# Optimization experiments

Measured on AMD Instinct MI355X. Metric: run time of the kernel, lower is better.

## Reference

```python
import jax, jax.numpy as jnp
import numpy as np

N = 16384          # input points
F = 128            # feature dim (x is (N, 3+F))
POOL = 4           # pooling_factor
M = N // POOL      # number of FPS query points
K = 16             # num_neighbors


def setup_inputs() -> dict:
    key = jax.random.key(0)
    x = jax.random.normal(key, (N, 3 + F), dtype=jnp.float32)
    return {"x": x}


def _fps(coords, m):
    """Furthest point sampling: coords (N,3) -> m indices. Deterministic start at 0."""
    n = coords.shape[0]

    def step(carry, _):
        min_d2, last = carry
        d2 = jnp.sum((coords - coords[last]) ** 2, axis=-1)  # (N,)
        min_d2 = jnp.minimum(min_d2, d2)
        nxt = jnp.argmax(min_d2).astype(jnp.int32)
        return (min_d2, nxt), nxt

    init = (jnp.full((n,), jnp.inf, dtype=coords.dtype), jnp.int32(0))
    _, idxs = jax.lax.scan(step, init, None, length=m - 1)
    return jnp.concatenate([jnp.zeros((1,), dtype=jnp.int32), idxs])


def reference(x):
    coords = x[:, :3]                          # (N,3)
    fps_idx = _fps(coords, M)                  # (M,)
    q_points = coords[fps_idx]                 # (M,3)

    # knn neighbor query: squared distances (M,N), take K nearest
    d2 = jnp.sum((q_points[:, None, :] - coords[None, :, :]) ** 2, axis=-1)
    _, nbr_idx = jax.lax.top_k(-d2, K)         # (M,K)

    s_feats = x[nbr_idx, 3:]                   # (M,K,F) gather
    pooled = jnp.max(s_feats, axis=1)          # feat_mapping='max' -> (M,F)
    return jnp.concatenate([q_points, pooled], axis=-1)  # (M, 3+F)
```

## Files before the change

### kernel.cpp

```cpp
#include <hip/hip_runtime.h>

#define N_PTS 16384
#define ROWF  131
#define M_OUT 4096
#define KNN   16
#define FPS_T 1024

typedef unsigned long long u64;
typedef float f32x2 __attribute__((ext_vector_type(2)));

template <int CTRL, int ROW_MASK>
__device__ __forceinline__ float fmax_dpp(float v) {
  const int p = __builtin_amdgcn_update_dpp(__float_as_int(v), __float_as_int(v),
                                            CTRL, ROW_MASK, 0xf, false);
  return fmaxf(v, __int_as_float(p));
}
template <int CTRL, int ROW_MASK>
__device__ __forceinline__ unsigned umin_dpp(unsigned v) {
  const unsigned p = (unsigned)__builtin_amdgcn_update_dpp((int)v, (int)v,
                                            CTRL, ROW_MASK, 0xf, false);
  return v < p ? v : p;
}

__global__ void prep_kernel(const float* __restrict__ x,
                            float4* __restrict__ coords4) {
  const int p = blockIdx.x * blockDim.x + threadIdx.x;
  if (p < N_PTS) {
    coords4[p] = make_float4(x[p * ROWF + 0], x[p * ROWF + 1],
                             x[p * ROWF + 2], 0.0f);
  }
}

#define REP16R(F) F(15) F(14) F(13) F(12) F(11) F(10) F(9) F(8) \
                  F(7) F(6) F(5) F(4) F(3) F(2) F(1) F(0)
#define REPP(F) F(0,0,1) F(1,2,3) F(2,4,5) F(3,6,7) \
                F(4,8,9) F(5,10,11) F(6,12,13) F(7,14,15)

__global__
__attribute__((amdgpu_flat_work_group_size(FPS_T, FPS_T)))
__attribute__((amdgpu_waves_per_eu(4, 4)))
void fps_kernel(const float4* __restrict__ coords4, float* __restrict__ out) {
#pragma clang fp contract(off)
  __shared__ float    s_wmax[2][16];
  __shared__ unsigned s_arg[2][16];
  const int tid = threadIdx.x, lane = tid & 63, wid = tid >> 6;

#define FPS_DECL(t,a,b) f32x2 PX##t, PY##t, PZ##t; float md##a, md##b;
  REPP(FPS_DECL)
#undef FPS_DECL

#define FPS_INIT(t,a,b) {                                                  \
    const float4 va = coords4[(a << 10) + tid];                            \
    const float4 vb = coords4[(b << 10) + tid];                            \
    PX##t = (f32x2){va.x, vb.x};                                           \
    PY##t = (f32x2){va.y, vb.y};                                           \
    PZ##t = (f32x2){va.z, vb.z};                                           \
    md##a = __int_as_float(0x7f800000);                                    \
    md##b = __int_as_float(0x7f800000); }
  REPP(FPS_INIT)
#undef FPS_INIT

  if (lane == 63) { s_arg[0][wid] = 0xFFFFFFFFu; s_arg[1][wid] = 0xFFFFFFFFu; }

  const float4 q0 = coords4[0];
  float qx = q0.x, qy = q0.y, qz = q0.z;
  if (tid == 0) { out[0] = qx; out[1] = qy; out[2] = qz; }

  for (int s = 1; s < M_OUT; ++s) {
    const int par = s & 1;
    const f32x2 QX = {qx, qx}, QY = {qy, qy}, QZ = {qz, qz};

#define FPS_UPD(t,a,b) {                                                   \
    const f32x2 dx = PX##t - QX;                                           \
    const f32x2 dy = PY##t - QY;                                           \
    const f32x2 dz = PZ##t - QZ;                                           \
    const f32x2 xx = dx * dx;                                              \
    const f32x2 yy = dy * dy;                                              \
    const f32x2 zz = dz * dz;                                              \
    const f32x2 ss = xx + yy;                                              \
    const f32x2 d2 = ss + zz;                                              \
    md##a = fminf(md##a, d2.x);                                            \
    md##b = fminf(md##b, d2.y); }
    REPP(FPS_UPD)
#undef FPS_UPD

    const float a0 = fmaxf(fmaxf(md0,  md1),  md2);
    const float a1 = fmaxf(fmaxf(md3,  md4),  md5);
    const float a2 = fmaxf(fmaxf(md6,  md7),  md8);
    const float a3 = fmaxf(fmaxf(md9,  md10), md11);
    const float a4 = fmaxf(fmaxf(md12, md13), md14);
    const float b0 = fmaxf(fmaxf(a0, a1), a2);
    const float b1 = fmaxf(fmaxf(a3, a4), md15);
    const float m  = fmaxf(b0, b1);

    float fm = m;
    fm = fmax_dpp<0xB1,  0xf>(fm);
    fm = fmax_dpp<0x4E,  0xf>(fm);
    fm = fmax_dpp<0x141, 0xf>(fm);
    fm = fmax_dpp<0x140, 0xf>(fm);
    fm = fmax_dpp<0x142, 0xa>(fm);
    fm = fmax_dpp<0x143, 0xc>(fm);

    if (lane == 63) s_wmax[par][wid] = fm;
    __syncthreads();

    if (lane == 63) s_arg[par ^ 1][wid] = 0xFFFFFFFFu;

    float bm = s_wmax[par][lane & 15];
    bm = fmax_dpp<0xB1,  0xf>(bm);
    bm = fmax_dpp<0x4E,  0xf>(bm);
    bm = fmax_dpp<0x141, 0xf>(bm);
    bm = fmax_dpp<0x140, 0xf>(bm);

    const int mwb = __builtin_amdgcn_readlane(__float_as_int(fm), 63);
    const int mmb = __builtin_amdgcn_readfirstlane(__float_as_int(bm));
    if (mwb == mmb) {
      const float mmv = __int_as_float(mmb);
      unsigned c = 0xFFFFu;
#define FPS_SCAN(j) c = (md##j == mmv) ? (unsigned)j : c;
      REP16R(FPS_SCAN)
#undef FPS_SCAN
      unsigned nic = (unsigned)tid + (c << 10);
      nic = umin_dpp<0xB1,  0xf>(nic);
      nic = umin_dpp<0x4E,  0xf>(nic);
      nic = umin_dpp<0x141, 0xf>(nic);
      nic = umin_dpp<0x140, 0xf>(nic);
      nic = umin_dpp<0x142, 0xa>(nic);
      nic = umin_dpp<0x143, 0xc>(nic);
      if (lane == 63) s_arg[par][wid] = nic;
    }
    __syncthreads();

    unsigned av = s_arg[par][lane & 15];
    av = umin_dpp<0xB1,  0xf>(av);
    av = umin_dpp<0x4E,  0xf>(av);
    av = umin_dpp<0x141, 0xf>(av);
    av = umin_dpp<0x140, 0xf>(av);

    const int oidx = (int)av;
    const float4 wpt = coords4[oidx];
    qx = wpt.x; qy = wpt.y; qz = wpt.z;
    if (tid == 0) {
      float* orow = out + (size_t)s * ROWF;
      orow[0] = qx; orow[1] = qy; orow[2] = qz;
    }
  }
}

__global__ __launch_bounds__(256)
void knn_pool_kernel(const float* __restrict__ x,
                     const float4* __restrict__ coords4,
                     float* __restrict__ out) {
  const int lane = threadIdx.x & 63;
  const int q = blockIdx.x * 4 + (threadIdx.x >> 6);

  const float qx = out[(size_t)q * ROWF + 0];
  const float qy = out[(size_t)q * ROWF + 1];
  const float qz = out[(size_t)q * ROWF + 2];

  u64 h[KNN];
#pragma unroll
  for (int k = 0; k < KNN; ++k) h[k] = ~0ULL;

  for (int c = lane; c < N_PTS; c += 64) {
    const float4 v = coords4[c];
    const float dx = v.x - qx, dy = v.y - qy, dz = v.z - qz;
    const float d2 = __fadd_rn(__fadd_rn(__fmul_rn(dx, dx), __fmul_rn(dy, dy)),
                               __fmul_rn(dz, dz));
    const u64 e = ((u64)__float_as_uint(d2) << 32) | (unsigned)c;
    if (e < h[KNN - 1]) {
#pragma unroll
      for (int k = KNN - 1; k >= 1; --k) {
        const u64 prev = h[k - 1];
        h[k] = (e < prev) ? prev : ((e < h[k]) ? e : h[k]);
      }
      h[0] = (e < h[0]) ? e : h[0];
    }
  }

  int nbr[KNN];
#pragma unroll
  for (int rr = 0; rr < KNN; ++rr) {
    u64 best = h[0];
#pragma unroll
    for (int off = 32; off; off >>= 1) {
      const u64 o = __shfl_xor(best, off);
      best = (o < best) ? o : best;
    }
    nbr[rr] = (int)(unsigned)(best & 0xffffffffULL);
    if (h[0] == best) {
#pragma unroll
      for (int k = 0; k < KNN - 1; ++k) h[k] = h[k + 1];
      h[KNN - 1] = ~0ULL;
    }
  }

  float a0 = __int_as_float(0xff800000), a1 = a0;
#pragma unroll
  for (int rr = 0; rr < KNN; ++rr) {
    const float* row = x + (size_t)nbr[rr] * ROWF + 3;
    a0 = fmaxf(a0, row[lane]);
    a1 = fmaxf(a1, row[lane + 64]);
  }
  float* orow = out + (size_t)q * ROWF + 3;
  orow[lane] = a0;
  orow[lane + 64] = a1;
}

extern "C" void kernel_launch(void* const* d_in, const int* in_sizes, int n_in,
                              void* d_out, int out_size, void* d_ws, size_t ws_size,
                              hipStream_t stream) {
  const float* x = (const float*)d_in[0];
  float* out = (float*)d_out;

  float4* coords4 = (float4*)d_ws;

  hipLaunchKernelGGL(prep_kernel, dim3(64), dim3(256), 0, stream, x, coords4);
  hipLaunchKernelGGL(fps_kernel, dim3(1), dim3(FPS_T), 0, stream, coords4, out);
  hipLaunchKernelGGL(knn_pool_kernel, dim3(M_OUT / 4), dim3(256), 0, stream,
                     x, coords4, out);
}
```

Before: 6.218 ms.

## Shrink FPS block to 4 waves with 64 points per thread in registers

The single-block furthest point sampling kernel drops from 1024 threads (16 waves) to 256 threads (4 waves), and each thread now holds 64 points in registers instead of 16. Cross-wave reductions through shared memory shrink from 16 to 4 entries, which cuts barrier and LDS latency on the serial per-step critical path. In exchange each thread does four times more distance and min work per step on only 4 waves (one per SIMD), so latency hiding is lower and register pressure is high.

```diff
diff --git a/kernel.cpp b/kernel.cpp
--- a/kernel.cpp
+++ b/kernel.cpp
@@ -4,7 +4,7 @@
 #define ROWF  131
 #define M_OUT 4096
 #define KNN   16
-#define FPS_T 1024
+#define FPS_T 256
 
 typedef unsigned long long u64;
 typedef float f32x2 __attribute__((ext_vector_type(2)));
@@ -31,18 +31,30 @@
   }
 }
 
-#define REP16R(F) F(15) F(14) F(13) F(12) F(11) F(10) F(9) F(8) \
+#define REP64R(F) F(63) F(62) F(61) F(60) F(59) F(58) F(57) F(56) \
+                  F(55) F(54) F(53) F(52) F(51) F(50) F(49) F(48) \
+                  F(47) F(46) F(45) F(44) F(43) F(42) F(41) F(40) \
+                  F(39) F(38) F(37) F(36) F(35) F(34) F(33) F(32) \
+                  F(31) F(30) F(29) F(28) F(27) F(26) F(25) F(24) \
+                  F(23) F(22) F(21) F(20) F(19) F(18) F(17) F(16) \
+                  F(15) F(14) F(13) F(12) F(11) F(10) F(9) F(8) \
                   F(7) F(6) F(5) F(4) F(3) F(2) F(1) F(0)
-#define REPP(F) F(0,0,1) F(1,2,3) F(2,4,5) F(3,6,7) \
-                F(4,8,9) F(5,10,11) F(6,12,13) F(7,14,15)
+#define REPP(F) F(0,0,1)    F(1,2,3)    F(2,4,5)    F(3,6,7) \
+                F(4,8,9)    F(5,10,11)  F(6,12,13)  F(7,14,15) \
+                F(8,16,17)  F(9,18,19)  F(10,20,21) F(11,22,23) \
+                F(12,24,25) F(13,26,27) F(14,28,29) F(15,30,31) \
+                F(16,32,33) F(17,34,35) F(18,36,37) F(19,38,39) \
+                F(20,40,41) F(21,42,43) F(22,44,45) F(23,46,47) \
+                F(24,48,49) F(25,50,51) F(26,52,53) F(27,54,55) \
+                F(28,56,57) F(29,58,59) F(30,60,61) F(31,62,63)
 
 __global__
 __attribute__((amdgpu_flat_work_group_size(FPS_T, FPS_T)))
-__attribute__((amdgpu_waves_per_eu(4, 4)))
+__attribute__((amdgpu_waves_per_eu(1, 1)))
 void fps_kernel(const float4* __restrict__ coords4, float* __restrict__ out) {
 #pragma clang fp contract(off)
-  __shared__ float    s_wmax[2][16];
-  __shared__ unsigned s_arg[2][16];
+  __shared__ float    s_wmax[2][4];
+  __shared__ unsigned s_arg[2][4];
   const int tid = threadIdx.x, lane = tid & 63, wid = tid >> 6;
 
 #define FPS_DECL(t,a,b) f32x2 PX##t, PY##t, PZ##t; float md##a, md##b;
@@ -50,8 +62,8 @@
 #undef FPS_DECL
 
 #define FPS_INIT(t,a,b) {                                                  \
-    const float4 va = coords4[(a << 10) + tid];                            \
-    const float4 vb = coords4[(b << 10) + tid];                            \
+    const float4 va = coords4[(a << 8) + tid];                             \
+    const float4 vb = coords4[(b << 8) + tid];                             \
     PX##t = (f32x2){va.x, vb.x};                                           \
     PY##t = (f32x2){va.y, vb.y};                                           \
     PZ##t = (f32x2){va.z, vb.z};                                           \
@@ -84,14 +96,38 @@
     REPP(FPS_UPD)
 #undef FPS_UPD
 
-    const float a0 = fmaxf(fmaxf(md0,  md1),  md2);
-    const float a1 = fmaxf(fmaxf(md3,  md4),  md5);
-    const float a2 = fmaxf(fmaxf(md6,  md7),  md8);
-    const float a3 = fmaxf(fmaxf(md9,  md10), md11);
-    const float a4 = fmaxf(fmaxf(md12, md13), md14);
-    const float b0 = fmaxf(fmaxf(a0, a1), a2);
-    const float b1 = fmaxf(fmaxf(a3, a4), md15);
-    const float m  = fmaxf(b0, b1);
+    const float g0  = fmaxf(fmaxf(md0,  md1),  md2);
+    const float g1  = fmaxf(fmaxf(md3,  md4),  md5);
+    const float g2  = fmaxf(fmaxf(md6,  md7),  md8);
+    const float g3  = fmaxf(fmaxf(md9,  md10), md11);
+    const float g4  = fmaxf(fmaxf(md12, md13), md14);
+    const float g5  = fmaxf(fmaxf(md15, md16), md17);
+    const float g6  = fmaxf(fmaxf(md18, md19), md20);
+    const float g7  = fmaxf(fmaxf(md21, md22), md23);
+    const float g8  = fmaxf(fmaxf(md24, md25), md26);
+    const float g9  = fmaxf(fmaxf(md27, md28), md29);
+    const float g10 = fmaxf(fmaxf(md30, md31), md32);
+    const float g11 = fmaxf(fmaxf(md33, md34), md35);
+    const float g12 = fmaxf(fmaxf(md36, md37), md38);
+    const float g13 = fmaxf(fmaxf(md39, md40), md41);
+    const float g14 = fmaxf(fmaxf(md42, md43), md44);
+    const float g15 = fmaxf(fmaxf(md45, md46), md47);
+    const float g16 = fmaxf(fmaxf(md48, md49), md50);
+    const float g17 = fmaxf(fmaxf(md51, md52), md53);
+    const float g18 = fmaxf(fmaxf(md54, md55), md56);
+    const float g19 = fmaxf(fmaxf(md57, md58), md59);
+    const float g20 = fmaxf(fmaxf(md60, md61), md62);
+    const float h0 = fmaxf(fmaxf(g0,  g1),  g2);
+    const float h1 = fmaxf(fmaxf(g3,  g4),  g5);
+    const float h2 = fmaxf(fmaxf(g6,  g7),  g8);
+    const float h3 = fmaxf(fmaxf(g9,  g10), g11);
+    const float h4 = fmaxf(fmaxf(g12, g13), g14);
+    const float h5 = fmaxf(fmaxf(g15, g16), g17);
+    const float h6 = fmaxf(fmaxf(g18, g19), g20);
+    const float k0 = fmaxf(fmaxf(h0, h1), h2);
+    const float k1 = fmaxf(fmaxf(h3, h4), h5);
+    const float k2 = fmaxf(h6, md63);
+    const float m  = fmaxf(fmaxf(k0, k1), k2);
 
     float fm = m;
     fm = fmax_dpp<0xB1,  0xf>(fm);
@@ -106,11 +142,9 @@
 
     if (lane == 63) s_arg[par ^ 1][wid] = 0xFFFFFFFFu;
 
-    float bm = s_wmax[par][lane & 15];
-    bm = fmax_dpp<0xB1,  0xf>(bm);
-    bm = fmax_dpp<0x4E,  0xf>(bm);
-    bm = fmax_dpp<0x141, 0xf>(bm);
-    bm = fmax_dpp<0x140, 0xf>(bm);
+    float bm = s_wmax[par][lane & 3];
+    bm = fmax_dpp<0xB1, 0xf>(bm);
+    bm = fmax_dpp<0x4E, 0xf>(bm);
 
     const int mwb = __builtin_amdgcn_readlane(__float_as_int(fm), 63);
     const int mmb = __builtin_amdgcn_readfirstlane(__float_as_int(bm));
@@ -118,9 +152,9 @@
       const float mmv = __int_as_float(mmb);
       unsigned c = 0xFFFFu;
 #define FPS_SCAN(j) c = (md##j == mmv) ? (unsigned)j : c;
-      REP16R(FPS_SCAN)
+      REP64R(FPS_SCAN)
 #undef FPS_SCAN
-      unsigned nic = (unsigned)tid + (c << 10);
+      unsigned nic = (unsigned)tid + (c << 8);
       nic = umin_dpp<0xB1,  0xf>(nic);
       nic = umin_dpp<0x4E,  0xf>(nic);
       nic = umin_dpp<0x141, 0xf>(nic);
@@ -131,11 +165,9 @@
     }
     __syncthreads();
 
-    unsigned av = s_arg[par][lane & 15];
-    av = umin_dpp<0xB1,  0xf>(av);
-    av = umin_dpp<0x4E,  0xf>(av);
-    av = umin_dpp<0x141, 0xf>(av);
-    av = umin_dpp<0x140, 0xf>(av);
+    unsigned av = s_arg[par][lane & 3];
+    av = umin_dpp<0xB1, 0xf>(av);
+    av = umin_dpp<0x4E, 0xf>(av);
 
     const int oidx = (int)av;
     const float4 wpt = coords4[oidx];
```

Result: slower. 7.456 ms (+19.9%).
